# Kernel tuning notes

Measured on AMD Instinct MI355X. Metric: run time of the kernel, lower is better.

The kernel has to match this reference:

```python
import jax, jax.numpy as jnp
import numpy as np

B, S, D = 2, 2048, 2048
N_HEADS, N_KV_HEADS = 16, 4
HEAD_DIM = D // N_HEADS  # 128
THETA = 10000.0
NEG_INF = -1e9


def setup_inputs() -> dict:
    key = jax.random.key(0)
    k1, k2, k3 = jax.random.split(key, 3)
    x = jax.random.normal(k1, (B, S, D), dtype=jnp.float32)
    w_qkv = jax.random.normal(k2, ((N_HEADS + 2 * N_KV_HEADS) * HEAD_DIM, D), dtype=jnp.float32) * (D ** -0.5)
    w_o = jax.random.normal(k3, (D, N_HEADS * HEAD_DIM), dtype=jnp.float32) * (D ** -0.5)
    return {"x": x, "w_qkv": w_qkv, "w_o": w_o}


def _apply_rope(q, k, seq_len, theta):
    # q: [B,S,Hq,hd], k: [B,S,Hk,hd]
    hd = q.shape[-1]
    t = jnp.arange(seq_len, dtype=jnp.float32)
    inv_freq = 1.0 / (theta ** (jnp.arange(0, hd, 2, dtype=jnp.float32) / hd))
    freqs = jnp.outer(t, inv_freq)            # [S, hd/2]
    cos = jnp.cos(freqs)[:, None, :]          # [S,1,hd/2] broadcasts over B,H
    sin = jnp.sin(freqs)[:, None, :]

    def rot(v):
        b, s, h, _ = v.shape
        v2 = v.reshape(b, s, h, hd // 2, 2)
        v0, v1 = v2[..., 0], v2[..., 1]
        out = jnp.stack([v0 * cos - v1 * sin, v0 * sin + v1 * cos], axis=-1)
        return out.reshape(b, s, h, hd)

    return rot(q), rot(k)


def reference(x, w_qkv, w_o):
    b, s, _ = x.shape
    q_size = N_HEADS * HEAD_DIM
    kv_size = N_KV_HEADS * HEAD_DIM
    # fused QKV projection
    qkv = jnp.einsum('bsd,od->bso', x, w_qkv)
    q = qkv[:, :, :q_size].reshape(b, s, N_HEADS, HEAD_DIM)
    k = qkv[:, :, q_size:q_size + kv_size].reshape(b, s, N_KV_HEADS, HEAD_DIM)
    v = qkv[:, :, q_size + kv_size:].reshape(b, s, N_KV_HEADS, HEAD_DIM)
    # RoPE
    q, k = _apply_rope(q, k, s, THETA)
    # GQA: repeat kv heads (repeat_interleave along head dim)
    rep = N_HEADS // N_KV_HEADS
    k = jnp.repeat(k, rep, axis=2)
    v = jnp.repeat(v, rep, axis=2)
    # [B,H,S,hd]
    q = q.transpose(0, 2, 1, 3)
    k = k.transpose(0, 2, 1, 3)
    v = v.transpose(0, 2, 1, 3)
    scale = HEAD_DIM ** -0.5
    scores = jnp.einsum('bhqd,bhkd->bhqk', q, k) * scale
    causal = jnp.tril(jnp.ones((s, s), dtype=bool))
    scores = jnp.where(causal[None, None], scores, NEG_INF)
    attn = jax.nn.softmax(scores, axis=-1)
    out = jnp.einsum('bhqk,bhkd->bhqd', attn, v)
    out = out.transpose(0, 2, 1, 3).reshape(b, s, N_HEADS * HEAD_DIM)
    return jnp.einsum('bsd,od->bso', out, w_o)
```

## Files before the change

kernel.cpp:

```cpp
#include <hip/hip_runtime.h>
#include <hip/hip_bf16.h>
#include <cstdint>
#include <cstddef>

typedef float f32x4 __attribute__((ext_vector_type(4)));
typedef float f32x16 __attribute__((ext_vector_type(16)));
typedef __bf16 bf16x8 __attribute__((ext_vector_type(8)));
typedef unsigned short us8v __attribute__((ext_vector_type(8)));
typedef unsigned short us4v __attribute__((ext_vector_type(4)));

constexpr int B_ = 2, S_ = 2048, D_ = 2048, NH = 16, NKV = 4, HD = 128;
constexpr int QKV_O = (NH + 2 * NKV) * HD;

__device__ __forceinline__ unsigned short f2b(float f) {
  union { float f; uint32_t u; } v{f};
  uint32_t r = v.u + 0x7fffu + ((v.u >> 16) & 1u);
  return (unsigned short)(r >> 16);
}

__device__ __forceinline__ uint32_t pk2(float a, float b) {
  union { __bf16 h[2]; uint32_t u; } v;
  v.h[0] = (__bf16)a; v.h[1] = (__bf16)b;
  return v.u;
}

__device__ __forceinline__ bf16x8 as_bf(us8v x) {
  union { us8v u; bf16x8 b; } v; v.u = x; return v.b;
}

__device__ __forceinline__ f32x4 mfma16(bf16x8 a, bf16x8 b, f32x4 c) {
  return __builtin_amdgcn_mfma_f32_16x16x32_bf16(a, b, c, 0, 0, 0);
}
__device__ __forceinline__ f32x16 mfma32(bf16x8 a, bf16x8 b, f32x16 c) {
  return __builtin_amdgcn_mfma_f32_32x32x16_bf16(a, b, c, 0, 0, 0);
}

__device__ __forceinline__ void gload_lds16(const unsigned short* g, unsigned short* l) {
  __builtin_amdgcn_global_load_lds(
      (const __attribute__((address_space(1))) unsigned int*)(uintptr_t)g,
      (__attribute__((address_space(3))) unsigned int*)(uintptr_t)l, 16, 0, 0);
}

__global__ void f2b_kernel(const float* __restrict__ in, unsigned short* __restrict__ out, int n4) {
  int i = blockIdx.x * blockDim.x + threadIdx.x;
  if (i >= n4) return;
  float4 v = reinterpret_cast<const float4*>(in)[i];
  us4v o;
  o[0] = f2b(v.x); o[1] = f2b(v.y); o[2] = f2b(v.z); o[3] = f2b(v.w);
  reinterpret_cast<us4v*>(out)[i] = o;
}

__global__ void rope_table_kernel(float* __restrict__ cs, float* __restrict__ sn) {
  int idx = blockIdx.x * blockDim.x + threadIdx.x;
  if (idx >= S_ * 64) return;
  int t = idx >> 6, i = idx & 63;
  float inv = __expf(-((float)(2 * i) / 128.0f) * 9.210340371976184f);
  float fr = (float)t * inv;
  cs[idx] = cosf(fr);
  sn[idx] = sinf(fr);
}

__global__ void rope_qk_kernel(const float* __restrict__ qkv, const float* __restrict__ cs,
                               const float* __restrict__ sn, unsigned short* __restrict__ Q,
                               unsigned short* __restrict__ K2) {
  int idx = blockIdx.x * blockDim.x + threadIdx.x;
  if (idx >= B_ * S_ * 20 * 64) return;
  int pr = idx & 63;
  int tmp = idx >> 6;
  int hh = tmp % 20; tmp /= 20;
  int s = tmp % S_;
  int b = tmp / S_;
  int off = (hh < 16) ? hh * HD : NH * HD + (hh - 16) * HD;
  float2 v = *reinterpret_cast<const float2*>(qkv + (size_t)(b * S_ + s) * QKV_O + off + 2 * pr);
  float c0 = cs[s * 64 + pr], s0 = sn[s * 64 + pr];
  float mult = (hh < 16) ? 0.12751744f : 1.0f;
  float o0 = (v.x * c0 - v.y * s0) * mult;
  float o1 = (v.x * s0 + v.y * c0) * mult;
  unsigned int packed = (unsigned)f2b(o0) | ((unsigned)f2b(o1) << 16);
  if (hh < 16) {
    *reinterpret_cast<unsigned*>(Q + (((size_t)(b * NH + hh) * S_ + s) * HD + 2 * pr)) = packed;
  } else {
    int bk = b * NKV + (hh - 16);
    size_t a = (((size_t)bk * 16 + (pr >> 2)) * S_ + s) * 8 + (pr & 3) * 2;
    *reinterpret_cast<unsigned*>(K2 + a) = packed;
  }
}

__global__ __launch_bounds__(128) void v8_kernel(const float* __restrict__ qkv,
                                                 unsigned short* __restrict__ V2) {
  int d = threadIdx.x;
  int g = blockIdx.x;
  int bk = blockIdx.y;
  const float* src = qkv + (size_t)((bk >> 2) * S_ + g * 8) * QKV_O + (NH + NKV) * HD +
                     (bk & 3) * HD + d;
  us8v o;
#pragma unroll
  for (int j = 0; j < 8; j++) o[j] = f2b(src[(size_t)j * QKV_O]);
  *reinterpret_cast<us8v*>(V2 + (((size_t)bk * 256 + g) * 128 + d) * 8) = o;
}

__global__ __launch_bounds__(512, 2) void gemm8p_kernel(const unsigned short* __restrict__ A,
                                                        const unsigned short* __restrict__ Bm,
                                                        float* __restrict__ C, int M, int N,
                                                        int K, int nbx) {
  __shared__ unsigned short LDS[65536];
  const int t = threadIdx.x;
  const int lane = t & 63, wid = t >> 6;
  const int wm = wid >> 2, wn = wid & 3;
  const int c = lane & 15, g4 = lane >> 4;
  const int cpx = gridDim.x >> 3;
  const int nid = (blockIdx.x & 7) * cpx + (blockIdx.x >> 3);
  const int m0 = (nid / nbx) * 256, n0 = (nid % nbx) * 256;

  const int sr = t >> 3, ss = t & 7;
  const int sg = ss ^ (sr & 7);
  const unsigned short* pa = A + (size_t)(m0 + sr) * K + sg * 8;
  const unsigned short* pb = Bm + (size_t)(n0 + sr) * K + sg * 8;
  unsigned short* ldw = (unsigned short*)&LDS[wid << 9];

  f32x4 acc[8][4] = {};
  bf16x8 bf[4][2];

#define STAGE_A(buf, j, kk0) \
  gload_lds16(pa + (size_t)(64 * (j)) * K + (kk0), ldw + (buf)*16384 + (j)*4096)
#define STAGE_B(buf, j, kk0) \
  gload_lds16(pb + (size_t)(64 * (j)) * K + (kk0), ldw + 32768 + (buf)*16384 + (j)*4096)

#define LDA(buf, m, kk) \
  as_bf(*reinterpret_cast<const us8v*>( \
      &LDS[(buf)*16384 + (wm * 128 + (m)*16 + c) * 64 + ((((kk) << 2) | g4) ^ (c & 7)) * 8]))
#define LDB(buf, n, kk) \
  as_bf(*reinterpret_cast<const us8v*>( \
      &LDS[32768 + (buf)*16384 + (wn * 64 + (n)*16 + c) * 64 + ((((kk) << 2) | g4) ^ (c & 7)) * 8]))

#pragma unroll
  for (int j = 0; j < 4; j++) STAGE_B(0, j, 0);
#pragma unroll
  for (int j = 0; j < 4; j++) STAGE_A(0, j, 0);
  asm volatile("s_waitcnt vmcnt(0)" ::: "memory");
  __builtin_amdgcn_s_barrier();

  const int NT = K >> 6;
  for (int tt = 0; tt < NT; ++tt) {
    const int cur = tt & 1, nxt = cur ^ 1;
    const int kn = (tt + 1) << 6;
    const bool st = (tt + 1) < NT;
    bf16x8 a00, a01, a10, a11;

#define MFMA_PAIR(mlo)                                    \
  __builtin_amdgcn_s_setprio(1);                          \
  _Pragma("unroll") for (int n = 0; n < 4; n++) {         \
    acc[(mlo)][n] = mfma16(a00, bf[n][0], acc[(mlo)][n]); \
    acc[(mlo) + 1][n] = mfma16(a10, bf[n][0], acc[(mlo) + 1][n]); \
    acc[(mlo)][n] = mfma16(a01, bf[n][1], acc[(mlo)][n]); \
    acc[(mlo) + 1][n] = mfma16(a11, bf[n][1], acc[(mlo) + 1][n]); \
  }                                                       \
  __builtin_amdgcn_s_setprio(0);

#pragma unroll
    for (int n = 0; n < 4; n++) { bf[n][0] = LDB(cur, n, 0); bf[n][1] = LDB(cur, n, 1); }
    a00 = LDA(cur, 0, 0); a01 = LDA(cur, 0, 1); a10 = LDA(cur, 1, 0); a11 = LDA(cur, 1, 1);
    if (st) { STAGE_B(nxt, 0, kn); STAGE_B(nxt, 1, kn); }
    __builtin_amdgcn_s_barrier();
    MFMA_PAIR(0)
    __builtin_amdgcn_s_barrier();
    a00 = LDA(cur, 2, 0); a01 = LDA(cur, 2, 1); a10 = LDA(cur, 3, 0); a11 = LDA(cur, 3, 1);
    if (st) { STAGE_B(nxt, 2, kn); STAGE_B(nxt, 3, kn); }
    asm volatile("s_waitcnt vmcnt(4)" ::: "memory");
    __builtin_amdgcn_s_barrier();
    MFMA_PAIR(2)
    __builtin_amdgcn_s_barrier();
    a00 = LDA(cur, 4, 0); a01 = LDA(cur, 4, 1); a10 = LDA(cur, 5, 0); a11 = LDA(cur, 5, 1);
    if (st) { STAGE_A(nxt, 0, kn); STAGE_A(nxt, 2, kn); }
    __builtin_amdgcn_s_barrier();
    MFMA_PAIR(4)
    __builtin_amdgcn_s_barrier();
    a00 = LDA(cur, 6, 0); a01 = LDA(cur, 6, 1); a10 = LDA(cur, 7, 0); a11 = LDA(cur, 7, 1);
    if (st) { STAGE_A(nxt, 1, kn); STAGE_A(nxt, 3, kn); }
    asm volatile("s_waitcnt vmcnt(2)" ::: "memory");
    __builtin_amdgcn_s_barrier();
    MFMA_PAIR(6)
    __builtin_amdgcn_s_barrier();
#undef MFMA_PAIR
  }

#pragma unroll
  for (int m = 0; m < 8; m++)
#pragma unroll
    for (int n = 0; n < 4; n++)
#pragma unroll
      for (int r = 0; r < 4; r++)
        C[(size_t)(m0 + wm * 128 + m * 16 + g4 * 4 + r) * N + n0 + wn * 64 + n * 16 + c] =
            acc[m][n][r];
#undef STAGE_A
#undef STAGE_B
#undef LDA
#undef LDB
}

__global__ __launch_bounds__(512, 2) void gemm8pn_kernel(const unsigned short* __restrict__ A,
                                                         const unsigned short* __restrict__ Bm,
                                                         float* __restrict__ C, int M, int N,
                                                         int K, int nbx) {
  __shared__ unsigned short LDS[49152];
  const int t = threadIdx.x;
  const int lane = t & 63, wid = t >> 6;
  const int wm = wid >> 2, wn = wid & 3;
  const int c = lane & 15, g4 = lane >> 4;
  const int cpx = gridDim.x >> 3;
  const int nid = (blockIdx.x & 7) * cpx + (blockIdx.x >> 3);
  const int m0 = (nid / nbx) * 256, n0 = (nid % nbx) * 128;

  const int sr = t >> 3, ss = t & 7;
  const int sg = ss ^ (sr & 7);
  const unsigned short* pa = A + (size_t)(m0 + sr) * K + sg * 8;
  const unsigned short* pb = Bm + (size_t)(n0 + sr) * K + sg * 8;
  unsigned short* ldw = (unsigned short*)&LDS[wid << 9];

  f32x4 acc[8][2] = {};
  bf16x8 bf[2][2];

#define STAGE_A(buf, j, kk0) \
  gload_lds16(pa + (size_t)(64 * (j)) * K + (kk0), ldw + (buf)*16384 + (j)*4096)
#define STAGE_B(buf, j, kk0) \
  gload_lds16(pb + (size_t)(64 * (j)) * K + (kk0), ldw + 32768 + (buf)*8192 + (j)*4096)

#define LDA(buf, m, kk) \
  as_bf(*reinterpret_cast<const us8v*>( \
      &LDS[(buf)*16384 + (wm * 128 + (m)*16 + c) * 64 + ((((kk) << 2) | g4) ^ (c & 7)) * 8]))
#define LDB(buf, n, kk) \
  as_bf(*reinterpret_cast<const us8v*>( \
      &LDS[32768 + (buf)*8192 + (wn * 32 + (n)*16 + c) * 64 + ((((kk) << 2) | g4) ^ (c & 7)) * 8]))

  STAGE_B(0, 0, 0); STAGE_B(0, 1, 0);
#pragma unroll
  for (int j = 0; j < 4; j++) STAGE_A(0, j, 0);
  asm volatile("s_waitcnt vmcnt(0)" ::: "memory");
  __builtin_amdgcn_s_barrier();

  const int NT = K >> 6;
  for (int tt = 0; tt < NT; ++tt) {
    const int cur = tt & 1, nxt = cur ^ 1;
    const int kn = (tt + 1) << 6;
    const bool st = (tt + 1) < NT;
    bf16x8 a00, a01, a10, a11;

#define MFMA_PAIR(mlo)                                    \
  __builtin_amdgcn_s_setprio(1);                          \
  _Pragma("unroll") for (int n = 0; n < 2; n++) {         \
    acc[(mlo)][n] = mfma16(a00, bf[n][0], acc[(mlo)][n]); \
    acc[(mlo) + 1][n] = mfma16(a10, bf[n][0], acc[(mlo) + 1][n]); \
    acc[(mlo)][n] = mfma16(a01, bf[n][1], acc[(mlo)][n]); \
    acc[(mlo) + 1][n] = mfma16(a11, bf[n][1], acc[(mlo) + 1][n]); \
  }                                                       \
  __builtin_amdgcn_s_setprio(0);

#pragma unroll
    for (int n = 0; n < 2; n++) { bf[n][0] = LDB(cur, n, 0); bf[n][1] = LDB(cur, n, 1); }
    a00 = LDA(cur, 0, 0); a01 = LDA(cur, 0, 1); a10 = LDA(cur, 1, 0); a11 = LDA(cur, 1, 1);
    if (st) STAGE_B(nxt, 0, kn);
    __builtin_amdgcn_s_barrier();
    MFMA_PAIR(0)
    __builtin_amdgcn_s_barrier();
    a00 = LDA(cur, 2, 0); a01 = LDA(cur, 2, 1); a10 = LDA(cur, 3, 0); a11 = LDA(cur, 3, 1);
    if (st) STAGE_B(nxt, 1, kn);
    asm volatile("s_waitcnt vmcnt(2)" ::: "memory");
    __builtin_amdgcn_s_barrier();
    MFMA_PAIR(2)
    __builtin_amdgcn_s_barrier();
    a00 = LDA(cur, 4, 0); a01 = LDA(cur, 4, 1); a10 = LDA(cur, 5, 0); a11 = LDA(cur, 5, 1);
    if (st) { STAGE_A(nxt, 0, kn); STAGE_A(nxt, 2, kn); }
    __builtin_amdgcn_s_barrier();
    MFMA_PAIR(4)
    __builtin_amdgcn_s_barrier();
    a00 = LDA(cur, 6, 0); a01 = LDA(cur, 6, 1); a10 = LDA(cur, 7, 0); a11 = LDA(cur, 7, 1);
    if (st) { STAGE_A(nxt, 1, kn); STAGE_A(nxt, 3, kn); }
    asm volatile("s_waitcnt vmcnt(2)" ::: "memory");
    __builtin_amdgcn_s_barrier();
    MFMA_PAIR(6)
    __builtin_amdgcn_s_barrier();
#undef MFMA_PAIR
  }

#pragma unroll
  for (int m = 0; m < 8; m++)
#pragma unroll
    for (int n = 0; n < 2; n++)
#pragma unroll
      for (int r = 0; r < 4; r++)
        C[(size_t)(m0 + wm * 128 + m * 16 + g4 * 4 + r) * N + n0 + wn * 32 + n * 16 + c] =
            acc[m][n][r];
#undef STAGE_A
#undef STAGE_B
#undef LDA
#undef LDB
}

__global__ __launch_bounds__(512, 2) void attn32_kernel(const unsigned short* __restrict__ Q,
                                                        const unsigned short* __restrict__ K2,
                                                        const unsigned short* __restrict__ V2,
                                                        unsigned short* __restrict__ O) {
  int t = threadIdx.x;
  int lane = t & 63, wid = t >> 6;
  int l31 = lane & 31, hi = lane >> 5;

  int id = blockIdx.x;
  int g = id & 7, s5 = id >> 3;
  int b = g >> 2, kvh = g & 3;
  int h = kvh * 4 + (s5 & 3);
  int bk = b * NKV + kvh;
  int a = (s5 >> 2) * 4 + (wid & 3);
  int tw = (wid >> 2) ? (63 - a) : a;
  int qw = tw * 32;

  const unsigned short* Qp = Q + ((size_t)(b * NH + h) * S_ + qw) * HD + (size_t)l31 * HD + hi * 8;
  const unsigned short* Kp = K2 + (((size_t)bk * 16 + hi) * S_ + l31) * 8;
  const unsigned short* Vp = V2 + (((size_t)bk * 256 + hi) * 128 + l31) * 8;

  bf16x8 qf[8];
#pragma unroll
  for (int kk = 0; kk < 8; kk++)
    qf[kk] = as_bf(*reinterpret_cast<const us8v*>(Qp + kk * 16));

  f32x16 oacc[4] = {};
  float mrow = -1e30f, lsum = 0.0f;

  bf16x8 kA[8], kB[8];

  auto loadK = [&](bf16x8(&kf)[8], int kv) {
    const unsigned short* kp = Kp + (size_t)kv * 8;
#pragma unroll
    for (int kk = 0; kk < 8; kk++)
      kf[kk] = as_bf(*reinterpret_cast<const us8v*>(kp + (size_t)kk * 2 * S_ * 8));
  };

  auto step = [&](bf16x8(&kf)[8], bf16x8(&kn)[8], int kv0) {
    bf16x8 vf[8];
    const unsigned short* vp = Vp + (size_t)kv0 * 128;
#pragma unroll
    for (int dt = 0; dt < 4; dt++) {
      vf[2 * dt] = as_bf(*reinterpret_cast<const us8v*>(vp + dt * 256));
      vf[2 * dt + 1] = as_bf(*reinterpret_cast<const us8v*>(vp + 2048 + dt * 256));
    }
    if (kv0 + 32 <= qw) loadK(kn, kv0 + 32);

    f32x16 sa = {}, sb = {};
    __builtin_amdgcn_s_setprio(1);
#pragma unroll
    for (int kk = 0; kk < 4; kk++) {
      sa = mfma32(kf[2 * kk], qf[2 * kk], sa);
      sb = mfma32(kf[2 * kk + 1], qf[2 * kk + 1], sb);
    }
    __builtin_amdgcn_s_setprio(0);
    f32x16 s = sa + sb;

    if (kv0 == qw) {
      int qg = qw + l31;
#pragma unroll
      for (int r = 0; r < 16; r++) {
        int kvg = kv0 + (r & 3) + 8 * (r >> 2) + 4 * hi;
        if (kvg > qg) s[r] = -1e30f;
      }
    }

    float pm = fmaxf(s[0], s[1]);
#pragma unroll
    for (int r = 2; r < 16; r++) pm = fmaxf(pm, s[r]);
    pm = fmaxf(pm, __shfl_xor(pm, 32));

    bool nore = __all(pm <= mrow + 11.54f) != 0;
    float mn = nore ? mrow : fmaxf(mrow, pm);
    float part = 0.0f;
    uint32_t w[8];
#pragma unroll
    for (int jj = 0; jj < 8; jj++) {
      float e0 = __builtin_amdgcn_exp2f(s[2 * jj] - mn);
      float e1 = __builtin_amdgcn_exp2f(s[2 * jj + 1] - mn);
      part += e0 + e1;
      w[jj] = pk2(e0, e1);
    }
    part += __shfl_xor(part, 32);
    if (nore) {
      lsum += part;
    } else {
      float alpha = __builtin_amdgcn_exp2f(mrow - mn);
      lsum = lsum * alpha + part;
      mrow = mn;
#pragma unroll
      for (int r = 0; r < 16; r++) {
        float af = __shfl(alpha, (r & 3) + 8 * (r >> 2) + 4 * hi);
#pragma unroll
        for (int dt = 0; dt < 4; dt++) oacc[dt][r] *= af;
      }
    }

    uint32_t sw[8];
#pragma unroll
    for (int jj = 0; jj < 8; jj++) sw[jj] = __shfl_xor(w[jj], 32);
    union { uint32_t u[4]; bf16x8 v; } pa0, pa1;
    if (hi == 0) {
      pa0.u[0] = w[0]; pa0.u[1] = w[1]; pa0.u[2] = sw[0]; pa0.u[3] = sw[1];
      pa1.u[0] = w[4]; pa1.u[1] = w[5]; pa1.u[2] = sw[4]; pa1.u[3] = sw[5];
    } else {
      pa0.u[0] = sw[2]; pa0.u[1] = sw[3]; pa0.u[2] = w[2]; pa0.u[3] = w[3];
      pa1.u[0] = sw[6]; pa1.u[1] = sw[7]; pa1.u[2] = w[6]; pa1.u[3] = w[7];
    }

    __builtin_amdgcn_s_setprio(1);
#pragma unroll
    for (int dt = 0; dt < 4; dt++) {
      oacc[dt] = mfma32(pa0.v, vf[2 * dt], oacc[dt]);
      oacc[dt] = mfma32(pa1.v, vf[2 * dt + 1], oacc[dt]);
    }
    __builtin_amdgcn_s_setprio(0);
  };

  loadK(kA, 0);
  int kv0 = 0;
  while (true) {
    step(kA, kB, kv0);
    kv0 += 32;
    if (kv0 > qw) break;
    step(kB, kA, kv0);
    kv0 += 32;
    if (kv0 > qw) break;
  }

  float il = 1.0f / lsum;
  unsigned short* Op = O + ((size_t)b * S_ + qw) * D_ + h * HD;
#pragma unroll
  for (int r = 0; r < 16; r++) {
    int row = (r & 3) + 8 * (r >> 2) + 4 * hi;
    float sc = __shfl(il, row);
#pragma unroll
    for (int dt = 0; dt < 4; dt++)
      Op[(size_t)row * D_ + dt * 32 + l31] = f2b(oacc[dt][r] * sc);
  }
}

extern "C" void kernel_launch(void* const* d_in, const int* in_sizes, int n_in, void* d_out,
                              int out_size, void* d_ws, size_t ws_size, hipStream_t stream) {
  const float* x = (const float*)d_in[0];
  const float* w_qkv = (const float*)d_in[1];
  const float* w_o = (const float*)d_in[2];
  float* out = (float*)d_out;

  char* ws = (char*)d_ws;
  size_t off = 0;
  auto alloc = [&](size_t bytes) -> void* {
    void* p = ws + off;
    off += (bytes + 255) & ~(size_t)255;
    return p;
  };
  const size_t nx = (size_t)B_ * S_ * D_;
  const size_t nwqkv = (size_t)QKV_O * D_;
  const size_t nwo = (size_t)D_ * D_;
  unsigned short* xb = (unsigned short*)alloc(nx * 2);
  unsigned short* wqkvb = (unsigned short*)alloc(nwqkv * 2);
  unsigned short* wob = (unsigned short*)alloc(nwo * 2);
  float* qkv = (float*)alloc((size_t)B_ * S_ * QKV_O * 4);
  unsigned short* Qb = (unsigned short*)alloc((size_t)B_ * NH * S_ * HD * 2);
  unsigned short* K2b = (unsigned short*)alloc((size_t)B_ * NKV * S_ * HD * 2);
  unsigned short* V2b = (unsigned short*)alloc((size_t)B_ * NKV * HD * S_ * 2);
  unsigned short* attnb = (unsigned short*)alloc((size_t)B_ * S_ * D_ * 2);
  float* cs = (float*)alloc((size_t)S_ * 64 * 4);
  float* sn = (float*)alloc((size_t)S_ * 64 * 4);

  f2b_kernel<<<dim3((nx / 4 + 255) / 256), 256, 0, stream>>>(x, xb, nx / 4);
  f2b_kernel<<<dim3((nwqkv / 4 + 255) / 256), 256, 0, stream>>>(w_qkv, wqkvb, nwqkv / 4);
  f2b_kernel<<<dim3((nwo / 4 + 255) / 256), 256, 0, stream>>>(w_o, wob, nwo / 4);
  rope_table_kernel<<<dim3((S_ * 64 + 255) / 256), 256, 0, stream>>>(cs, sn);

  gemm8p_kernel<<<dim3(192), 512, 0, stream>>>(xb, wqkvb, qkv, B_ * S_, QKV_O, D_, QKV_O / 256);

  rope_qk_kernel<<<dim3((B_ * S_ * 20 * 64 + 255) / 256), 256, 0, stream>>>(qkv, cs, sn, Qb, K2b);
  v8_kernel<<<dim3(S_ / 8, B_ * NKV), 128, 0, stream>>>(qkv, V2b);

  attn32_kernel<<<dim3(256), 512, 0, stream>>>(Qb, K2b, V2b, attnb);

  gemm8pn_kernel<<<dim3(256), 512, 0, stream>>>(attnb, wob, out, B_ * S_, D_, D_, D_ / 128);
}
```

Baseline: 205.9 us.

## Split causal attention KV range across wave pairs and merge partial softmax in LDS

New measurement: 581.3 us. 182% more time.

```diff
diff --git a/kernel.cpp b/kernel.cpp
--- a/kernel.cpp
+++ b/kernel.cpp
@@ -296,10 +296,14 @@
 #undef LDB
 }
 
-__global__ __launch_bounds__(512, 2) void attn32_kernel(const unsigned short* __restrict__ Q,
+__global__ __launch_bounds__(512, 4) void attn32_kernel(const unsigned short* __restrict__ Q,
                                                         const unsigned short* __restrict__ K2,
                                                         const unsigned short* __restrict__ V2,
                                                         unsigned short* __restrict__ O) {
+  __shared__ float stO[4][4][16][64];
+  __shared__ float stM[4][64];
+  __shared__ float stL[4][64];
+
   int t = threadIdx.x;
   int lane = t & 63, wid = t >> 6;
   int l31 = lane & 31, hi = lane >> 5;
@@ -309,8 +313,15 @@
   int b = g >> 2, kvh = g & 3;
   int h = kvh * 4 + (s5 & 3);
   int bk = b * NKV + kvh;
-  int a = (s5 >> 2) * 4 + (wid & 3);
-  int tw = (wid >> 2) ? (63 - a) : a;
+  int pp = s5 >> 2;
+  int j = wid & 3;
+  int aidx = pp * 2 + (j >> 1);
+  int base = (j & 1) ? (63 - aidx) : aidx;
+  bool isHi = (wid >> 2) != 0;
+  int tw = isHi ? (63 - base) : base;
+  int H = (tw + 1) >> 1;
+  int kb = isHi ? H : 0;
+  int ke = isHi ? tw : (H - 1);
   int qw = tw * 32;
 
   const unsigned short* Qp = Q + ((size_t)(b * NH + h) * S_ + qw) * HD + (size_t)l31 * HD + hi * 8;
@@ -334,6 +345,7 @@
       kf[kk] = as_bf(*reinterpret_cast<const us8v*>(kp + (size_t)kk * 2 * S_ * 8));
   };
 
+  int kend = ke * 32;
   auto step = [&](bf16x8(&kf)[8], bf16x8(&kn)[8], int kv0) {
     bf16x8 vf[8];
     const unsigned short* vp = Vp + (size_t)kv0 * 128;
@@ -342,7 +354,7 @@
       vf[2 * dt] = as_bf(*reinterpret_cast<const us8v*>(vp + dt * 256));
       vf[2 * dt + 1] = as_bf(*reinterpret_cast<const us8v*>(vp + 2048 + dt * 256));
     }
-    if (kv0 + 32 <= qw) loadK(kn, kv0 + 32);
+    if (kv0 + 32 <= kend) loadK(kn, kv0 + 32);
 
     f32x16 sa = {}, sb = {};
     __builtin_amdgcn_s_setprio(1);
@@ -415,26 +427,48 @@
     __builtin_amdgcn_s_setprio(0);
   };
 
-  loadK(kA, 0);
-  int kv0 = 0;
-  while (true) {
-    step(kA, kB, kv0);
-    kv0 += 32;
-    if (kv0 > qw) break;
-    step(kB, kA, kv0);
-    kv0 += 32;
-    if (kv0 > qw) break;
+  if (kb <= ke) {
+    loadK(kA, kb * 32);
+    int kv0 = kb * 32;
+    while (true) {
+      step(kA, kB, kv0);
+      kv0 += 32;
+      if (kv0 > kend) break;
+      step(kB, kA, kv0);
+      kv0 += 32;
+      if (kv0 > kend) break;
+    }
   }
 
-  float il = 1.0f / lsum;
+  if (!isHi) {
+#pragma unroll
+    for (int dt = 0; dt < 4; dt++)
+#pragma unroll
+      for (int r = 0; r < 16; r++) stO[wid][dt][r][lane] = oacc[dt][r];
+    stM[wid][lane] = mrow;
+    stL[wid][lane] = lsum;
+  }
+  __syncthreads();
+  if (!isHi) return;
+
+  int p = (wid & 3) ^ 1;
+  float m1 = stM[p][lane], l1 = stL[p][lane];
+  float mm = fmaxf(mrow, m1);
+  float fo = __builtin_amdgcn_exp2f(mrow - mm), fp = __builtin_amdgcn_exp2f(m1 - mm);
+  float lf = lsum * fo + l1 * fp;
+  float il = 1.0f / lf;
   unsigned short* Op = O + ((size_t)b * S_ + qw) * D_ + h * HD;
 #pragma unroll
   for (int r = 0; r < 16; r++) {
     int row = (r & 3) + 8 * (r >> 2) + 4 * hi;
-    float sc = __shfl(il, row);
-#pragma unroll
-    for (int dt = 0; dt < 4; dt++)
-      Op[(size_t)row * D_ + dt * 32 + l31] = f2b(oacc[dt][r] * sc);
+    float fo_r = __shfl(fo, row);
+    float fp_r = __shfl(fp, row);
+    float il_r = __shfl(il, row);
+#pragma unroll
+    for (int dt = 0; dt < 4; dt++) {
+      float v = (oacc[dt][r] * fo_r + stO[p][dt][r][lane] * fp_r) * il_r;
+      Op[(size_t)row * D_ + dt * 32 + l31] = f2b(v);
+    }
   }
 }
 
@@ -476,7 +510,7 @@
   rope_qk_kernel<<<dim3((B_ * S_ * 20 * 64 + 255) / 256), 256, 0, stream>>>(qkv, cs, sn, Qb, K2b);
   v8_kernel<<<dim3(S_ / 8, B_ * NKV), 128, 0, stream>>>(qkv, V2b);
 
-  attn32_kernel<<<dim3(256), 512, 0, stream>>>(Qb, K2b, V2b, attnb);
+  attn32_kernel<<<dim3(512), 512, 0, stream>>>(Qb, K2b, V2b, attnb);
 
   gemm8pn_kernel<<<dim3(256), 512, 0, stream>>>(attnb, wob, out, B_ * S_, D_, D_, D_ / 128);
 }
```
